# Performance work log

Hardware: AMD Instinct MI355X
Metric: run time of the kernel (lower is better)

The kernel has to match this reference:

```python
import jax, jax.numpy as jnp
import numpy as np

NUM_TIMES = 1024  # times are drawn from [0, 1024), used as fixed segment count
N = 16777216


def setup_inputs() -> dict:
    key = jax.random.key(0)
    k1, k2, k3 = jax.random.split(key, 3)
    outs = jax.random.normal(k1, (N,), dtype=jnp.float32)
    T_E = jax.random.randint(k2, (N,), 0, 2, dtype=jnp.int32)
    T_T = jax.random.randint(k3, (N,), 0, NUM_TIMES, dtype=jnp.int32)
    return {"outs": outs, "T_E": T_E, "T_T": T_T}


def reference(outs, T_E, T_T):
    # E[E > 0] = 1  -> binary event indicator
    E = (T_E > 0).astype(outs.dtype)
    # Y_label_T = |T_T| ; integer times act directly as segment ids
    seg_ids = jnp.abs(T_T)
    Obs = jnp.sum(E)
    # log of running sum of hazards: log(cumsum(exp(yhat)))
    y_hat_cumsum = jnp.log(jnp.cumsum(jnp.exp(outs)))
    # original segment_max initializes accumulator at 0, so it is clipped below at 0;
    # jnp.maximum also neutralizes -inf fill for empty segments (count=0 there anyway)
    seg_max = jnp.maximum(
        jax.ops.segment_max(y_hat_cumsum, seg_ids, num_segments=NUM_TIMES), 0.0
    )
    seg_cnt = jax.ops.segment_sum(E, seg_ids, num_segments=NUM_TIMES)
    loss_s2 = jnp.sum(seg_max * seg_cnt)
    loss_s1 = jnp.sum(outs * E)
    return (loss_s2 - loss_s1) / Obs
```

## Files before the change

kernel.cpp:

```cpp
#include <hip/hip_runtime.h>

#define NUM_SEGS 1024
#define CHUNK_LOG 13
#define CHUNK (1 << CHUNK_LOG)
#define SUBCH 4
#define SUPER (CHUNK * SUBCH)
#define BLK 1024
#define NWAVE (BLK / 64)
#define NBATCH 8
#define PDEPTH 2
#define SEGBLK 256
#define SEGWAVES (SEGBLK / 64)

__device__ __forceinline__ float waveReduceSumF(float v) {
#pragma unroll
    for (int off = 32; off > 0; off >>= 1) v += __shfl_down(v, off, 64);
    return v;
}
__device__ __forceinline__ double waveReduceSumD(double v) {
#pragma unroll
    for (int off = 32; off > 0; off >>= 1) v += __shfl_down(v, off, 64);
    return v;
}
__device__ __forceinline__ unsigned waveReduceSumU(unsigned v) {
#pragma unroll
    for (int off = 32; off > 0; off >>= 1) v += __shfl_down(v, off, 64);
    return v;
}
__device__ __forceinline__ int waveReduceMaxI(int v) {
#pragma unroll
    for (int off = 32; off > 0; off >>= 1) {
        const int o = __shfl_down(v, off, 64);
        v = o > v ? o : v;
    }
    return v;
}

__global__ __launch_bounds__(BLK, 8) void pass1_kernel(
    const float* __restrict__ outs, const int* __restrict__ te,
    const int* __restrict__ tt, int N, int nChunks,
    float* __restrict__ csums, unsigned short* __restrict__ hist_part,
    float* __restrict__ e1part, unsigned* __restrict__ obspart) {
    __shared__ unsigned hist[NUM_SEGS];
    __shared__ float redC[SUBCH][NWAVE];
    __shared__ float redF[NWAVE];
    __shared__ unsigned redU[NWAVE];

    for (int t = threadIdx.x; t < NUM_SEGS; t += BLK) hist[t] = 0u;
    __syncthreads();

    const int lane = threadIdx.x & 63;
    const int wid = threadIdx.x >> 6;
    const int bid = (int)blockIdx.x;
    const int superBase = bid * SUPER;

    float sE[SUBCH] = {0.f, 0.f, 0.f, 0.f};
    float sumOE = 0.f;
    unsigned cntE = 0u;

    if (superBase + SUPER <= N) {
        const int i0 = superBase + ((int)threadIdx.x << 2);
        float4 O[PDEPTH];
        int4 E[PDEPTH], S[PDEPTH];

#define LOADB(b, sl)                                                        \
    do {                                                                    \
        const int _i = i0 + (b) * (BLK * 4);                                \
        O[sl] = *reinterpret_cast<const float4*>(outs + _i);                \
        E[sl] = *reinterpret_cast<const int4*>(te + _i);                    \
        S[sl] = *reinterpret_cast<const int4*>(tt + _i);                    \
    } while (0)

#pragma unroll
        for (int b = 0; b < PDEPTH; ++b) LOADB(b, b);

#pragma unroll
        for (int b = 0; b < NBATCH; ++b) {
            if (b + PDEPTH < NBATCH) LOADB(b + PDEPTH, (b + PDEPTH) % PDEPTH);
            __builtin_amdgcn_sched_barrier(0);
            {
                const int sl = b % PDEPTH;
                const float4 o = O[sl];
                const int4 ev = E[sl];
                const int4 sv = S[sl];
                sE[b >> 1] += (__expf(o.x) + __expf(o.y)) +
                              (__expf(o.z) + __expf(o.w));
                const int s0 = sv.x < 0 ? -sv.x : sv.x;
                const int s1 = sv.y < 0 ? -sv.y : sv.y;
                const int s2 = sv.z < 0 ? -sv.z : sv.z;
                const int s3 = sv.w < 0 ? -sv.w : sv.w;
                if (ev.x > 0) { cntE++; sumOE += o.x; atomicAdd(&hist[s0], 1u); }
                if (ev.y > 0) { cntE++; sumOE += o.y; atomicAdd(&hist[s1], 1u); }
                if (ev.z > 0) { cntE++; sumOE += o.z; atomicAdd(&hist[s2], 1u); }
                if (ev.w > 0) { cntE++; sumOE += o.w; atomicAdd(&hist[s3], 1u); }
            }
        }
#undef LOADB

#pragma unroll
        for (int k = 0; k < SUBCH; ++k) {
            const float w = waveReduceSumF(sE[k]);
            if (lane == 0) redC[k][wid] = w;
        }
    } else {
        if (lane == 0) {
#pragma unroll
            for (int k = 0; k < SUBCH; ++k) redC[k][wid] = 0.f;
        }
        for (int k = 0; k < SUBCH; ++k) {
            const int cbase = superBase + k * CHUNK;
            if (cbase >= N) break;
            const int end = (cbase + CHUNK < N) ? cbase + CHUNK : N;
            float s = 0.f;
            for (int i = cbase + (int)threadIdx.x; i < end; i += BLK) {
                const float o = outs[i];
                const int e = te[i];
                int sg = tt[i]; sg = sg < 0 ? -sg : sg;
                s += __expf(o);
                if (e > 0) { cntE++; sumOE += o; atomicAdd(&hist[sg], 1u); }
            }
            const float w = waveReduceSumF(s);
            if (lane == 0) redC[k][wid] = w;
        }
    }

    {
        const float wOE = waveReduceSumF(sumOE);
        const unsigned wC = waveReduceSumU(cntE);
        if (lane == 0) { redF[wid] = wOE; redU[wid] = wC; }
    }

    __syncthreads();

    for (int t = threadIdx.x; t < NUM_SEGS; t += BLK)
        hist_part[(size_t)bid * NUM_SEGS + t] = (unsigned short)hist[t];

    if (threadIdx.x == 0) {
        const int c0 = superBase >> CHUNK_LOG;
#pragma unroll
        for (int k = 0; k < SUBCH; ++k) {
            const int cbase = superBase + k * CHUNK;
            if (cbase < N) {
                float cs = 0.f;
#pragma unroll
                for (int j = 0; j < NWAVE; ++j) cs += redC[k][j];
                csums[c0 + k] = cs;
            }
        }
        float oe = 0.f; unsigned c = 0u;
#pragma unroll
        for (int j = 0; j < NWAVE; ++j) { oe += redF[j]; c += redU[j]; }
        e1part[bid] = oe;
        obspart[bid] = c;
    }
}

__global__ __launch_bounds__(SEGBLK) void seg_final_kernel(
    const float* __restrict__ outs, const int* __restrict__ tt,
    const float* __restrict__ csums, const unsigned short* __restrict__ hist_part,
    const float* __restrict__ e1part, const unsigned* __restrict__ obspart,
    float* __restrict__ out, int N, int nChunks, int nSuper) {
    __shared__ double redD[SEGWAVES];
    __shared__ float redF[SEGWAVES];
    __shared__ int redI[SEGWAVES];
    __shared__ unsigned redObs[SEGWAVES];
    __shared__ unsigned redCnt[SEGWAVES];
    __shared__ int s_li;
    __shared__ unsigned s_cnt;

    const int t = (int)blockIdx.x;
    const int tid = (int)threadIdx.x;
    const int lane = tid & 63, wid = tid >> 6;

    {
        unsigned ob = 0u;
        for (int b = tid; b < nSuper; b += SEGBLK) ob += obspart[b];
        ob = waveReduceSumU(ob);
        if (lane == 0) redObs[wid] = ob;
    }

    if (t == 0) {
        double p = 0.0;
        for (int b = tid; b < nSuper; b += SEGBLK) p += (double)e1part[b];
        p = waveReduceSumD(p);
        if (lane == 0) redD[wid] = p;
        __syncthreads();
        if (tid == 0) {
            double L1 = 0.0, Obs = 0.0;
#pragma unroll
            for (int j = 0; j < SEGWAVES; ++j) {
                L1 += redD[j];
                Obs += (double)redObs[j];
            }
            atomicAdd(out, (float)(-L1 / Obs));
        }
        __syncthreads();
    }

    {
        unsigned c = 0u;
        for (int b = tid; b < nSuper; b += SEGBLK)
            c += (unsigned)hist_part[(size_t)b * NUM_SEGS + t];
        c = waveReduceSumU(c);
        if (lane == 0) redCnt[wid] = c;
    }
    __syncthreads();
    if (tid == 0) {
        unsigned c = 0u;
#pragma unroll
        for (int j = 0; j < SEGWAVES; ++j) c += redCnt[j];
        s_cnt = c;
    }
    __syncthreads();
    const unsigned cnt = s_cnt;
    if (cnt == 0u) return;

    int c = nChunks - 1;
    int LI = -1;
    for (;;) {
        const int base = c << CHUNK_LOG;
        const int end = (base + CHUNK < N) ? base + CHUNK : N;
        const int span = end - base;
        const int qspan = span & ~3;
        int li = -1;
        for (int i = base + (tid << 2); i < base + qspan; i += SEGBLK * 4) {
            const int4 sv = *reinterpret_cast<const int4*>(tt + i);
            const int s0 = sv.x < 0 ? -sv.x : sv.x;
            const int s1 = sv.y < 0 ? -sv.y : sv.y;
            const int s2 = sv.z < 0 ? -sv.z : sv.z;
            const int s3 = sv.w < 0 ? -sv.w : sv.w;
            if (s3 == t) li = i + 3;
            else if (s2 == t) li = i + 2;
            else if (s1 == t) li = i + 1;
            else if (s0 == t) li = i;
        }
        for (int i = base + qspan + tid; i < end; i += SEGBLK) {
            int s = tt[i]; s = s < 0 ? -s : s;
            if (s == t && i > li) li = i;
        }
        li = waveReduceMaxI(li);
        if (lane == 0) redI[wid] = li;
        __syncthreads();
        if (tid == 0) {
            int m = redI[0];
#pragma unroll
            for (int j = 1; j < SEGWAVES; ++j) m = redI[j] > m ? redI[j] : m;
            s_li = m;
        }
        __syncthreads();
        LI = s_li;
        if (LI >= 0 || --c < 0) break;
    }
    if (LI < 0) return;

    {
        double p = 0.0;
        for (int j = tid; j < c; j += SEGBLK) p += (double)csums[j];
        p = waveReduceSumD(p);
        if (lane == 0) redD[wid] = p;
    }

    {
        const int base = c << CHUNK_LOG;
        float fs = 0.f;
        for (int i = base + tid; i <= LI; i += SEGBLK) fs += __expf(outs[i]);
        fs = waveReduceSumF(fs);
        if (lane == 0) redF[wid] = fs;
    }
    __syncthreads();
    if (tid == 0) {
        double pre = 0.0, Obs = 0.0;
        float fsum = 0.f;
#pragma unroll
        for (int j = 0; j < SEGWAVES; ++j) {
            pre += redD[j];
            fsum += redF[j];
            Obs += (double)redObs[j];
        }
        double sm = log(pre + (double)fsum);
        if (sm < 0.0) sm = 0.0;
        atomicAdd(out, (float)(sm * (double)cnt / Obs));
    }
}

extern "C" void kernel_launch(void* const* d_in, const int* in_sizes, int n_in,
                              void* d_out, int out_size, void* d_ws, size_t ws_size,
                              hipStream_t stream) {
    const float* outs = (const float*)d_in[0];
    const int* te = (const int*)d_in[1];
    const int* tt = (const int*)d_in[2];
    const int N = in_sizes[0];
    float* out = (float*)d_out;

    const int nChunks = (N + CHUNK - 1) / CHUNK;
    const int nSuper = (N + SUPER - 1) / SUPER;

    char* ws = (char*)d_ws;
    float* d_csums = (float*)ws;
    unsigned short* d_histp = (unsigned short*)(d_csums + nChunks);
    float* d_e1 = (float*)(d_histp + (size_t)nSuper * NUM_SEGS);
    unsigned* d_obsp = (unsigned*)(d_e1 + nSuper);

    pass1_kernel<<<nSuper, BLK, 0, stream>>>(outs, te, tt, N, nChunks, d_csums,
                                             d_histp, d_e1, d_obsp);
    seg_final_kernel<<<NUM_SEGS, SEGBLK, 0, stream>>>(
        outs, tt, d_csums, d_histp, d_e1, d_obsp, out, N, nChunks, nSuper);
}
```

Before: 220.6 us.

## Stage pass1 inputs through LDS with async global_load_lds double buffering

Replaces the register-prefetched float4 loads in pass1 with per-wave double-buffered LDS staging via global_load_lds, using explicit vmcnt waits. The block shrinks from 1024 to 256 threads, each block now covers two 8K chunks instead of four, and each wave owns a contiguous 4096-element region. The aim is deeper in-flight memory traffic with fewer registers and better latency hiding for a bandwidth-bound pass. In exchange it adds LDS pressure, relies on a hand-written waitcnt being correct, and roughly doubles the number of per-block histogram partials that the final kernel must read.

```diff
diff --git a/kernel.cpp b/kernel.cpp
--- a/kernel.cpp
+++ b/kernel.cpp
@@ -3,14 +3,19 @@
 #define NUM_SEGS 1024
 #define CHUNK_LOG 13
 #define CHUNK (1 << CHUNK_LOG)
-#define SUBCH 4
+#define SUBCH 2
 #define SUPER (CHUNK * SUBCH)
-#define BLK 1024
+#define BLK 256
 #define NWAVE (BLK / 64)
-#define NBATCH 8
-#define PDEPTH 2
+#define STAGE 256
+#define NSTAGE 16
 #define SEGBLK 256
 #define SEGWAVES (SEGBLK / 64)
+
+#define GLOAD_LDS(gptr, lptr)                                                  \
+    __builtin_amdgcn_global_load_lds(                                          \
+        (const __attribute__((address_space(1))) void*)(gptr),                 \
+        (__attribute__((address_space(3))) void*)(lptr), 16, 0, 0)
 
 __device__ __forceinline__ float waveReduceSumF(float v) {
 #pragma unroll
@@ -36,55 +41,60 @@
     return v;
 }
 
-__global__ __launch_bounds__(BLK, 8) void pass1_kernel(
+__global__ __launch_bounds__(BLK, 4) void pass1_kernel(
     const float* __restrict__ outs, const int* __restrict__ te,
     const int* __restrict__ tt, int N, int nChunks,
     float* __restrict__ csums, unsigned short* __restrict__ hist_part,
     float* __restrict__ e1part, unsigned* __restrict__ obspart) {
     __shared__ unsigned hist[NUM_SEGS];
-    __shared__ float redC[SUBCH][NWAVE];
+    __shared__ float stgO[NWAVE][2][STAGE];
+    __shared__ int stgE[NWAVE][2][STAGE];
+    __shared__ int stgT[NWAVE][2][STAGE];
+    __shared__ float redK[SUBCH][NWAVE];
     __shared__ float redF[NWAVE];
     __shared__ unsigned redU[NWAVE];
 
-    for (int t = threadIdx.x; t < NUM_SEGS; t += BLK) hist[t] = 0u;
-    __syncthreads();
-
-    const int lane = threadIdx.x & 63;
-    const int wid = threadIdx.x >> 6;
+    const int tid = (int)threadIdx.x;
+    const int lane = tid & 63;
+    const int wid = tid >> 6;
     const int bid = (int)blockIdx.x;
     const int superBase = bid * SUPER;
 
-    float sE[SUBCH] = {0.f, 0.f, 0.f, 0.f};
+    for (int t = tid; t < NUM_SEGS; t += BLK) hist[t] = 0u;
+    if (tid < SUBCH * NWAVE) redK[tid >> 2][tid & 3] = 0.f;
+    __syncthreads();
+
+    float sumExp = 0.f;
     float sumOE = 0.f;
     unsigned cntE = 0u;
 
     if (superBase + SUPER <= N) {
-        const int i0 = superBase + ((int)threadIdx.x << 2);
-        float4 O[PDEPTH];
-        int4 E[PDEPTH], S[PDEPTH];
-
-#define LOADB(b, sl)                                                        \
-    do {                                                                    \
-        const int _i = i0 + (b) * (BLK * 4);                                \
-        O[sl] = *reinterpret_cast<const float4*>(outs + _i);                \
-        E[sl] = *reinterpret_cast<const int4*>(te + _i);                    \
-        S[sl] = *reinterpret_cast<const int4*>(tt + _i);                    \
+        const int wbase = superBase + (wid << 12);
+        const int l4 = lane << 2;
+
+#define ISSUE_STAGE(j, buf)                                                    \
+    do {                                                                       \
+        const int _sb = wbase + (j) * STAGE;                                   \
+        GLOAD_LDS(outs + _sb + l4, &stgO[wid][buf][0]);                        \
+        GLOAD_LDS(te + _sb + l4, &stgE[wid][buf][0]);                          \
+        GLOAD_LDS(tt + _sb + l4, &stgT[wid][buf][0]);                          \
     } while (0)
 
-#pragma unroll
-        for (int b = 0; b < PDEPTH; ++b) LOADB(b, b);
-
-#pragma unroll
-        for (int b = 0; b < NBATCH; ++b) {
-            if (b + PDEPTH < NBATCH) LOADB(b + PDEPTH, (b + PDEPTH) % PDEPTH);
+        ISSUE_STAGE(0, 0);
+#pragma unroll
+        for (int j = 0; j < NSTAGE; ++j) {
+            const int buf = j & 1;
+            if (j + 1 < NSTAGE) ISSUE_STAGE(j + 1, (j + 1) & 1);
+            __builtin_amdgcn_sched_barrier(0);
+            if (j + 1 < NSTAGE) asm volatile("s_waitcnt vmcnt(3)");
+            else                asm volatile("s_waitcnt vmcnt(0)");
             __builtin_amdgcn_sched_barrier(0);
             {
-                const int sl = b % PDEPTH;
-                const float4 o = O[sl];
-                const int4 ev = E[sl];
-                const int4 sv = S[sl];
-                sE[b >> 1] += (__expf(o.x) + __expf(o.y)) +
-                              (__expf(o.z) + __expf(o.w));
+                const float4 o = *reinterpret_cast<const float4*>(&stgO[wid][buf][l4]);
+                const int4 ev = *reinterpret_cast<const int4*>(&stgE[wid][buf][l4]);
+                const int4 sv = *reinterpret_cast<const int4*>(&stgT[wid][buf][l4]);
+                sumExp += (__expf(o.x) + __expf(o.y)) +
+                          (__expf(o.z) + __expf(o.w));
                 const int s0 = sv.x < 0 ? -sv.x : sv.x;
                 const int s1 = sv.y < 0 ? -sv.y : sv.y;
                 const int s2 = sv.z < 0 ? -sv.z : sv.z;
@@ -95,24 +105,17 @@
                 if (ev.w > 0) { cntE++; sumOE += o.w; atomicAdd(&hist[s3], 1u); }
             }
         }
-#undef LOADB
-
-#pragma unroll
-        for (int k = 0; k < SUBCH; ++k) {
-            const float w = waveReduceSumF(sE[k]);
-            if (lane == 0) redC[k][wid] = w;
-        }
+#undef ISSUE_STAGE
+
+        const float w = waveReduceSumF(sumExp);
+        if (lane == 0) redK[wid >> 1][wid] = w;
     } else {
-        if (lane == 0) {
-#pragma unroll
-            for (int k = 0; k < SUBCH; ++k) redC[k][wid] = 0.f;
-        }
         for (int k = 0; k < SUBCH; ++k) {
             const int cbase = superBase + k * CHUNK;
             if (cbase >= N) break;
             const int end = (cbase + CHUNK < N) ? cbase + CHUNK : N;
             float s = 0.f;
-            for (int i = cbase + (int)threadIdx.x; i < end; i += BLK) {
+            for (int i = cbase + tid; i < end; i += BLK) {
                 const float o = outs[i];
                 const int e = te[i];
                 int sg = tt[i]; sg = sg < 0 ? -sg : sg;
@@ -120,7 +123,7 @@
                 if (e > 0) { cntE++; sumOE += o; atomicAdd(&hist[sg], 1u); }
             }
             const float w = waveReduceSumF(s);
-            if (lane == 0) redC[k][wid] = w;
+            if (lane == 0 && w != 0.f) atomicAdd(&redK[k][0], w);
         }
     }
 
@@ -132,10 +135,10 @@
 
     __syncthreads();
 
-    for (int t = threadIdx.x; t < NUM_SEGS; t += BLK)
+    for (int t = tid; t < NUM_SEGS; t += BLK)
         hist_part[(size_t)bid * NUM_SEGS + t] = (unsigned short)hist[t];
 
-    if (threadIdx.x == 0) {
+    if (tid == 0) {
         const int c0 = superBase >> CHUNK_LOG;
 #pragma unroll
         for (int k = 0; k < SUBCH; ++k) {
@@ -143,7 +146,7 @@
             if (cbase < N) {
                 float cs = 0.f;
 #pragma unroll
-                for (int j = 0; j < NWAVE; ++j) cs += redC[k][j];
+                for (int j = 0; j < NWAVE; ++j) cs += redK[k][j];
                 csums[c0 + k] = cs;
             }
         }
```

Result: slower. 235.0 us (+6.5%).
